# Optimization experiments

Hardware: AMD Instinct MI355X
Metric: run time of the kernel (lower is better)

## Reference

```python
import jax, jax.numpy as jnp
import numpy as np

N = 100000   # num_nodes
E = 1250000  # num_edges
D = 64       # embedding_dim
L = 3        # num_layers


def setup_inputs() -> dict:
    key = jax.random.key(0)
    k1, k2, k3, k4 = jax.random.split(key, 4)
    edge_index = jax.random.randint(k1, (2, E), 0, N, dtype=jnp.int64)
    edge_label_index = jax.random.randint(k2, (2, E), 0, N, dtype=jnp.int64)
    # xavier_uniform init of Embedding(N, D)
    bound = float(np.sqrt(6.0 / (N + D)))
    emb_weight = jax.random.uniform(k3, (N, D), jnp.float32, -bound, bound)
    alpha = jnp.full((L + 1,), 1.0 / (L + 1), dtype=jnp.float32)
    return {"edge_index": edge_index, "edge_label_index": edge_label_index,
            "emb_weight": emb_weight, "alpha": alpha}


def reference(edge_index, edge_label_index, emb_weight, alpha):
    src, dst = edge_index[0], edge_index[1]
    n = emb_weight.shape[0]
    # gcn_norm (LGConv, no self-loops): deg over destination, sym normalization
    deg = jax.ops.segment_sum(jnp.ones(src.shape[0], emb_weight.dtype), dst, num_segments=n)
    dis = jnp.where(deg > 0, jax.lax.rsqrt(jnp.where(deg > 0, deg, 1.0)), 0.0)
    w = dis[src] * dis[dst]  # [E]

    weights = jax.nn.softmax(alpha)  # [L+1]
    x = emb_weight
    out = x * weights[0]
    for i in range(L):
        # LGConv: out[dst] += norm * x[src]
        x = jax.ops.segment_sum(w[:, None] * x[src], dst, num_segments=n)
        out = out + x * weights[i + 1]

    # predict_link_embedding: per-edge dot product
    return (out[edge_label_index[0]] * out[edge_label_index[1]]).sum(axis=-1)
```

## Files before the change

kernel.cpp:

```cpp
#include <hip/hip_runtime.h>
#include <math.h>

#define DIM 64
#define PART_T 4096
#define BK_SHIFT 9
#define BK_SPAN 512
#define BK_CAP 8192
#define BK_PAD 2048
#define BK_REG (BK_CAP + BK_PAD)

typedef _Float16 half8 __attribute__((ext_vector_type(8)));


__device__ __forceinline__ half8 shfl_xor_h8(half8 v, int mask) {
    int4 iv;
    __builtin_memcpy(&iv, &v, 16);
    iv.x = __shfl_xor(iv.x, mask, 64);
    iv.y = __shfl_xor(iv.y, mask, 64);
    iv.z = __shfl_xor(iv.z, mask, 64);
    iv.w = __shfl_xor(iv.w, mask, 64);
    half8 r;
    __builtin_memcpy(&r, &iv, 16);
    return r;
}

__device__ __forceinline__ half8 dpp_ror8_h8(half8 v) {
    int4 iv;
    __builtin_memcpy(&iv, &v, 16);
    int4 r;
    r.x = __builtin_amdgcn_update_dpp(0, iv.x, 0x128, 0xF, 0xF, true);
    r.y = __builtin_amdgcn_update_dpp(0, iv.y, 0x128, 0xF, 0xF, true);
    r.z = __builtin_amdgcn_update_dpp(0, iv.z, 0x128, 0xF, 0xF, true);
    r.w = __builtin_amdgcn_update_dpp(0, iv.w, 0x128, 0xF, 0xF, true);
    half8 out;
    __builtin_memcpy(&out, &r, 16);
    return out;
}

__device__ __forceinline__ float dpp_sum8_f32(float v) {
    int x = __float_as_int(v);
    v += __int_as_float(__builtin_amdgcn_update_dpp(0, x, 0xB1, 0xF, 0xF, true));
    x = __float_as_int(v);
    v += __int_as_float(__builtin_amdgcn_update_dpp(0, x, 0x4E, 0xF, 0xF, true));
    x = __float_as_int(v);
    v += __int_as_float(__builtin_amdgcn_update_dpp(0, x, 0x141, 0xF, 0xF, true));
    return v;
}

__device__ __forceinline__ int wave_incl_scan(int v) {
    int lane = threadIdx.x & 63;
    #pragma unroll
    for (int d = 1; d < 64; d <<= 1) {
        int n = __shfl_up(v, d, 64);
        if (lane >= d) v += n;
    }
    return v;
}

__device__ __forceinline__ int block_scan_excl(int v, int* wsum) {
    int incl = wave_incl_scan(v);
    int w = threadIdx.x >> 6;
    if ((threadIdx.x & 63) == 63) wsum[w] = incl;
    __syncthreads();
    int offset = 0;
    #pragma unroll
    for (int i = 0; i < 3; ++i) offset += (i < w) ? wsum[i] : 0;
    return offset + incl - v;
}


__global__ void init_kernel(int* __restrict__ gcursor, int K) {
    int t = threadIdx.x;
    if (t < K) gcursor[t] = t * BK_CAP;
}


__global__ void part_kernel(const int* __restrict__ src, const int* __restrict__ dst,
                            int* __restrict__ gcursor, unsigned int* __restrict__ part,
                            int E, int K) {
    __shared__ unsigned int tmp_rec[PART_T];
    __shared__ unsigned int reord[PART_T];
    __shared__ unsigned char tmp_bkt[PART_T];
    __shared__ unsigned char tmp_bkt2[PART_T];
    __shared__ int hist[256];
    __shared__ int lstart[256];
    __shared__ int cursor[256];
    __shared__ int gbase[256];
    __shared__ int wsum[4];
    int t = threadIdx.x;
    int tile = blockIdx.x * PART_T;
    int n = E - tile; if (n > PART_T) n = PART_T;

    hist[t] = 0;
    __syncthreads();

    for (int i = t; i < n; i += 256) {
        int s = src[tile + i];
        int d = dst[tile + i];
        int b = d >> BK_SHIFT;
        tmp_rec[i] = (unsigned int)s | ((unsigned int)(d & (BK_SPAN - 1)) << 17);
        tmp_bkt[i] = (unsigned char)b;
        atomicAdd(&hist[b], 1);
    }
    __syncthreads();

    int hv = hist[t];
    int excl = block_scan_excl(hv, wsum);
    lstart[t] = excl;
    cursor[t] = excl;
    if (t < K && hv > 0) gbase[t] = atomicAdd(&gcursor[t], hv);
    __syncthreads();

    for (int i = t; i < n; i += 256) {
        int b = tmp_bkt[i];
        int r = atomicAdd(&cursor[b], 1);
        reord[r] = tmp_rec[i];
        tmp_bkt2[r] = (unsigned char)b;
    }
    __syncthreads();

    for (int i = t; i < n; i += 256) {
        int b = tmp_bkt2[i];
        part[gbase[b] + (i - lstart[b])] = reord[i];
    }
}


__global__ void csr_kernel(const unsigned int* __restrict__ part, const int* __restrict__ gcursor,
                           int2* __restrict__ prange, int* __restrict__ csr_src,
                           float* __restrict__ dis, int N) {
    __shared__ int h[BK_SPAN];
    __shared__ int pfx[BK_SPAN + 1];
    __shared__ int wsum[4];
    int b = blockIdx.x;
    int t = threadIdx.x;
    int pbase = b * BK_CAP;
    int cnt   = gcursor[b] - pbase;
    int qbase = b * BK_REG;
    int nodeBase = b << BK_SHIFT;

    h[t] = 0; h[t + 256] = 0;
    __syncthreads();

    for (int j = t; j < cnt; j += 256) {
        unsigned int rec = part[pbase + j];
        atomicAdd(&h[rec >> 17], 1);
    }
    __syncthreads();

    int d0 = h[2 * t], d1 = h[2 * t + 1];
    {
        int i0 = nodeBase + 2 * t, i1 = i0 + 1;
        if (i0 < N) dis[i0] = d0 > 0 ? 1.0f / sqrtf((float)d0) : 0.0f;
        if (i1 < N) dis[i1] = d1 > 0 ? 1.0f / sqrtf((float)d1) : 0.0f;
    }
    int p0 = (d0 + 3) & ~3;
    int p1 = (d1 + 3) & ~3;
    int excl = block_scan_excl(p0 + p1, wsum);
    pfx[2 * t]     = excl;
    pfx[2 * t + 1] = excl + p0;
    h[2 * t]       = excl;
    h[2 * t + 1]   = excl + p0;
    if (t == 255) pfx[BK_SPAN] = excl + p0 + p1;
    __syncthreads();

    #pragma unroll
    for (int k = 0; k < 2; ++k) {
        int i = t + k * 256;
        int idx = nodeBase + i;
        if (idx < N) prange[idx] = make_int2(qbase + pfx[i], qbase + pfx[i + 1]);
    }
    __syncthreads();

    for (int j = t; j < cnt; j += 256) {
        unsigned int rec = part[pbase + j];
        int dl = (int)(rec >> 17);
        int s  = (int)(rec & 0x1FFFFu);
        int p = atomicAdd(&h[dl], 1);
        csr_src[qbase + p] = s;
    }
    __syncthreads();

    #pragma unroll
    for (int k = 0; k < 2; ++k) {
        int i = t + k * 256;
        int endp = pfx[i + 1];
        for (int p = h[i]; p < endp; ++p) csr_src[qbase + p] = N;
    }
}


__global__ void conv_kernel(const float* __restrict__ emb, const float* __restrict__ dis,
                            half8* __restrict__ g0, half8* __restrict__ g1,
                            half8* __restrict__ g2, int n8, int N) {
    int i = blockIdx.x * blockDim.x + threadIdx.x;
    if (i < 8) {
        half8 z = (half8)(_Float16)0;
        g0[(size_t)N * 8 + i] = z;
        g1[(size_t)N * 8 + i] = z;
        g2[(size_t)N * 8 + i] = z;
    }
    if (i >= n8) return;
    int v = i >> 3;
    float d = dis[v];
    const float4* e4 = (const float4*)emb;
    float4 a = e4[2 * i], b = e4[2 * i + 1];
    half8 h;
    h[0] = (_Float16)(d * a.x); h[1] = (_Float16)(d * a.y);
    h[2] = (_Float16)(d * a.z); h[3] = (_Float16)(d * a.w);
    h[4] = (_Float16)(d * b.x); h[5] = (_Float16)(d * b.y);
    h[6] = (_Float16)(d * b.z); h[7] = (_Float16)(d * b.w);
    g0[i] = h;
}


__device__ __forceinline__ void softmax4(const float* __restrict__ alpha, float* w) {
    float a0 = alpha[0], a1 = alpha[1], a2 = alpha[2], a3 = alpha[3];
    float m = fmaxf(fmaxf(a0, a1), fmaxf(a2, a3));
    float e0 = expf(a0 - m), e1 = expf(a1 - m), e2 = expf(a2 - m), e3 = expf(a3 - m);
    float s = 1.0f / (e0 + e1 + e2 + e3);
    w[0] = e0 * s; w[1] = e1 * s; w[2] = e2 * s; w[3] = e3 * s;
}

__global__ void spmm_kernel(const int2* __restrict__ prange, const int* __restrict__ csr_src,
                            const float* __restrict__ dis,
                            const half8* __restrict__ gin, half8* __restrict__ gout, int N) {
    int lane = threadIdx.x & 63;
    int wave = blockIdx.x * (blockDim.x >> 6) + (threadIdx.x >> 6);
    int v = wave * 2 + (lane >> 5);
    int slot = (lane >> 3) & 3;
    int sub  = lane & 7;
    bool valid = v < N;
    int beg = 0, end = 0;
    if (valid) { int2 pr = prange[v]; beg = pr.x; end = pr.y; }
    const int4* csr4 = (const int4*)csr_src;
    half8 acc0 = (half8)(_Float16)0;
    half8 acc1 = (half8)(_Float16)0;
    for (int j = beg + slot * 4; j < end; j += 16) {
        int4 c = csr4[j >> 2];
        acc0 = acc0 + gin[c.x * 8 + sub];
        acc1 = acc1 + gin[c.y * 8 + sub];
        acc0 = acc0 + gin[c.z * 8 + sub];
        acc1 = acc1 + gin[c.w * 8 + sub];
    }
    half8 acc = acc0 + acc1;
    acc = acc + dpp_ror8_h8(acc);
    acc = acc + shfl_xor_h8(acc, 16);
    if (valid && (lane & 31) < 8) {
        float d = dis[v];
        float d2 = d * d;
        half8 o;
        #pragma unroll
        for (int k = 0; k < 8; ++k) o[k] = (_Float16)(d2 * (float)acc[k]);
        gout[v * 8 + sub] = o;
    }
}

__global__ void spmm_final_kernel(const int2* __restrict__ prange, const int* __restrict__ csr_src,
                                  const float* __restrict__ dis,
                                  const float* __restrict__ emb, const half8* __restrict__ g1,
                                  const half8* __restrict__ g2, half8* __restrict__ out,
                                  const float* __restrict__ alpha, int N) {
    int lane = threadIdx.x & 63;
    int wave = blockIdx.x * (blockDim.x >> 6) + (threadIdx.x >> 6);
    int v = wave * 2 + (lane >> 5);
    int slot = (lane >> 3) & 3;
    int sub  = lane & 7;
    bool valid = v < N;
    int beg = 0, end = 0;
    if (valid) { int2 pr = prange[v]; beg = pr.x; end = pr.y; }
    const int4* csr4 = (const int4*)csr_src;
    half8 acc0 = (half8)(_Float16)0;
    half8 acc1 = (half8)(_Float16)0;
    for (int j = beg + slot * 4; j < end; j += 16) {
        int4 c = csr4[j >> 2];
        acc0 = acc0 + g2[c.x * 8 + sub];
        acc1 = acc1 + g2[c.y * 8 + sub];
        acc0 = acc0 + g2[c.z * 8 + sub];
        acc1 = acc1 + g2[c.w * 8 + sub];
    }
    half8 acc = acc0 + acc1;
    acc = acc + dpp_ror8_h8(acc);
    acc = acc + shfl_xor_h8(acc, 16);
    if (valid && (lane & 31) < 8) {
        float w[4];
        softmax4(alpha, w);
        float d  = dis[v];
        float iv = d > 0.0f ? 1.0f / d : 0.0f;
        const float4* e4 = (const float4*)emb;
        float4 ea = e4[v * 16 + sub * 2];
        float4 eb = e4[v * 16 + sub * 2 + 1];
        half8 h1 = g1[v * 8 + sub];
        half8 h2 = g2[v * 8 + sub];
        float ef[8] = {ea.x, ea.y, ea.z, ea.w, eb.x, eb.y, eb.z, eb.w};
        half8 o;
        #pragma unroll
        for (int k = 0; k < 8; ++k) {
            float x1 = (float)h1[k] * iv;
            float x2 = (float)h2[k] * iv;
            float x3 = d * (float)acc[k];
            float val = w[0] * ef[k] + w[1] * x1 + w[2] * x2 + w[3] * x3;
            o[k] = (_Float16)val;
        }
        out[v * 8 + sub] = o;
    }
}

__global__ void dot_kernel(const int* __restrict__ a, const int* __restrict__ b,
                           const half8* __restrict__ out, float* __restrict__ res, int E) {
    long long g = (long long)blockIdx.x * blockDim.x + threadIdx.x;
    int e   = (int)(g >> 3);
    int sub = (int)(g & 7);
    if (e >= E) return;
    int ia = a[e];
    int ib = b[e];
    half8 va = out[ia * 8 + sub];
    half8 vb = out[ib * 8 + sub];
#if __has_builtin(__builtin_amdgcn_fdot2)
    float v = 0.f;
    v = __builtin_amdgcn_fdot2(__builtin_shufflevector(va, va, 0, 1),
                               __builtin_shufflevector(vb, vb, 0, 1), v, false);
    v = __builtin_amdgcn_fdot2(__builtin_shufflevector(va, va, 2, 3),
                               __builtin_shufflevector(vb, vb, 2, 3), v, false);
    v = __builtin_amdgcn_fdot2(__builtin_shufflevector(va, va, 4, 5),
                               __builtin_shufflevector(vb, vb, 4, 5), v, false);
    v = __builtin_amdgcn_fdot2(__builtin_shufflevector(va, va, 6, 7),
                               __builtin_shufflevector(vb, vb, 6, 7), v, false);
#else
    float v = 0.f;
    #pragma unroll
    for (int k = 0; k < 8; ++k) v += (float)va[k] * (float)vb[k];
#endif
    v = dpp_sum8_f32(v);
    if (sub == 0) res[e] = v;
}


static inline size_t align256(size_t x) { return (x + 255) & ~(size_t)255; }

extern "C" void kernel_launch(void* const* d_in, const int* in_sizes, int n_in,
                              void* d_out, int out_size, void* d_ws, size_t ws_size,
                              hipStream_t stream) {
    const int* edge_index = (const int*)d_in[0];
    const int* edge_label = (const int*)d_in[1];
    const float* emb      = (const float*)d_in[2];
    const float* alpha    = (const float*)d_in[3];

    const int E = in_sizes[0] / 2;
    const int N = in_sizes[2] / DIM;
    const int K = (N + BK_SPAN - 1) >> BK_SHIFT;

    const int* src = edge_index;
    const int* dst = edge_index + E;
    const int* la  = edge_label;
    const int* lb  = edge_label + E;

    char* ws = (char*)d_ws;
    size_t off = 0;
    float* dis     = (float*)(ws + off); off = align256(off + (size_t)N * 4);
    int2*  prange  = (int2*)(ws + off);  off = align256(off + (size_t)N * 8);
    int*   gcursor = (int*)(ws + off);   off = align256(off + (size_t)256 * 4);
    unsigned int* part = (unsigned int*)(ws + off); off = align256(off + (size_t)K * BK_CAP * 4);
    int*   csr_src = (int*)(ws + off);   off = align256(off + (size_t)K * BK_REG * 4);
    half8* g0      = (half8*)(ws + off); off = align256(off + (size_t)(N + 1) * DIM * 2);
    half8* g1      = (half8*)(ws + off); off = align256(off + (size_t)(N + 1) * DIM * 2);
    half8* g2      = (half8*)(ws + off); off = align256(off + (size_t)(N + 1) * DIM * 2);
    half8* outbuf  = g0;
    (void)ws_size;

    const int B = 256;
    const int gridT = (E + PART_T - 1) / PART_T;

    init_kernel<<<1, B, 0, stream>>>(gcursor, K);

    part_kernel<<<gridT, B, 0, stream>>>(src, dst, gcursor, part, E, K);

    csr_kernel<<<K, B, 0, stream>>>(part, gcursor, prange, csr_src, dis, N);

    const int n8 = N * DIM / 8;
    conv_kernel<<<(n8 + B - 1) / B, B, 0, stream>>>(emb, dis, g0, g1, g2, n8, N);

    const int nodesPerBlock = (B / 64) * 2;
    const int gridS = (N + nodesPerBlock - 1) / nodesPerBlock;
    spmm_kernel<<<gridS, B, 0, stream>>>(prange, csr_src, dis, g0, g1, N);
    spmm_kernel<<<gridS, B, 0, stream>>>(prange, csr_src, dis, g1, g2, N);
    spmm_final_kernel<<<gridS, B, 0, stream>>>(prange, csr_src, dis, emb, g1, g2,
                                               outbuf, alpha, N);

    const long long dthreads = (long long)E * 8;
    const int gridD = (int)((dthreads + B - 1) / B);
    dot_kernel<<<gridD, B, 0, stream>>>(la, lb, outbuf, (float*)d_out, E);
}
```

Before: 232.5 us.

## Replace bucket partition CSR build with global atomic degree count and placement

Replaces the two-pass shared-memory bucket partition (part_kernel + csr_kernel) with a global atomic degree histogram, a per-bucket prefix kernel fused with the fp16 embedding conversion, and an atomic scatter placement of sources into CSR slots. This removes the intermediate partition buffer and one pass over the edges, and folds the separate conversion kernel into the prefix kernel. In exchange it relies on 1.25M global atomics over random destinations, twice, which may contend more than the shared-memory version. Neighbor order within a row becomes nondeterministic, and the fixed 10240-entry region per 512-node bucket could overflow if degrees are skewed.

```diff
diff --git a/kernel.cpp b/kernel.cpp
--- a/kernel.cpp
+++ b/kernel.cpp
@@ -2,12 +2,9 @@
 #include <math.h>
 
 #define DIM 64
-#define PART_T 4096
 #define BK_SHIFT 9
 #define BK_SPAN 512
-#define BK_CAP 8192
-#define BK_PAD 2048
-#define BK_REG (BK_CAP + BK_PAD)
+#define BK_REG 10240
 
 typedef _Float16 half8 __attribute__((ext_vector_type(8)));
 
@@ -69,98 +66,52 @@
 }
 
 
-__global__ void init_kernel(int* __restrict__ gcursor, int K) {
-    int t = threadIdx.x;
-    if (t < K) gcursor[t] = t * BK_CAP;
-}
-
-
-__global__ void part_kernel(const int* __restrict__ src, const int* __restrict__ dst,
-                            int* __restrict__ gcursor, unsigned int* __restrict__ part,
-                            int E, int K) {
-    __shared__ unsigned int tmp_rec[PART_T];
-    __shared__ unsigned int reord[PART_T];
-    __shared__ unsigned char tmp_bkt[PART_T];
-    __shared__ unsigned char tmp_bkt2[PART_T];
-    __shared__ int hist[256];
-    __shared__ int lstart[256];
-    __shared__ int cursor[256];
-    __shared__ int gbase[256];
-    __shared__ int wsum[4];
-    int t = threadIdx.x;
-    int tile = blockIdx.x * PART_T;
-    int n = E - tile; if (n > PART_T) n = PART_T;
-
-    hist[t] = 0;
-    __syncthreads();
-
-    for (int i = t; i < n; i += 256) {
-        int s = src[tile + i];
-        int d = dst[tile + i];
-        int b = d >> BK_SHIFT;
-        tmp_rec[i] = (unsigned int)s | ((unsigned int)(d & (BK_SPAN - 1)) << 17);
-        tmp_bkt[i] = (unsigned char)b;
-        atomicAdd(&hist[b], 1);
-    }
-    __syncthreads();
-
-    int hv = hist[t];
-    int excl = block_scan_excl(hv, wsum);
-    lstart[t] = excl;
-    cursor[t] = excl;
-    if (t < K && hv > 0) gbase[t] = atomicAdd(&gcursor[t], hv);
-    __syncthreads();
-
-    for (int i = t; i < n; i += 256) {
-        int b = tmp_bkt[i];
-        int r = atomicAdd(&cursor[b], 1);
-        reord[r] = tmp_rec[i];
-        tmp_bkt2[r] = (unsigned char)b;
-    }
-    __syncthreads();
-
-    for (int i = t; i < n; i += 256) {
-        int b = tmp_bkt2[i];
-        part[gbase[b] + (i - lstart[b])] = reord[i];
-    }
-}
-
-
-__global__ void csr_kernel(const unsigned int* __restrict__ part, const int* __restrict__ gcursor,
-                           int2* __restrict__ prange, int* __restrict__ csr_src,
-                           float* __restrict__ dis, int N) {
-    __shared__ int h[BK_SPAN];
+__global__ void zero_kernel(int* __restrict__ degcur, half8* __restrict__ g0,
+                            half8* __restrict__ g1, half8* __restrict__ g2, int N) {
+    int i = blockIdx.x * blockDim.x + threadIdx.x;
+    if (i < N) degcur[i] = 0;
+    if (blockIdx.x == 0 && threadIdx.x < 8) {
+        half8 z = (half8)(_Float16)0;
+        g0[(size_t)N * 8 + threadIdx.x] = z;
+        g1[(size_t)N * 8 + threadIdx.x] = z;
+        g2[(size_t)N * 8 + threadIdx.x] = z;
+    }
+}
+
+
+__global__ void deg_kernel(const int* __restrict__ dst, int* __restrict__ degcur, int E) {
+    int e = blockIdx.x * blockDim.x + threadIdx.x;
+    if (e < E) atomicAdd(&degcur[dst[e]], 1);
+}
+
+
+__global__ void prefix_conv_kernel(int* __restrict__ degcur, float* __restrict__ dis,
+                                   int2* __restrict__ prange, int* __restrict__ csr_src,
+                                   const float* __restrict__ emb, half8* __restrict__ g0,
+                                   int N) {
     __shared__ int pfx[BK_SPAN + 1];
+    __shared__ float sdis[BK_SPAN];
     __shared__ int wsum[4];
     int b = blockIdx.x;
     int t = threadIdx.x;
-    int pbase = b * BK_CAP;
-    int cnt   = gcursor[b] - pbase;
+    int nodeBase = b << BK_SHIFT;
     int qbase = b * BK_REG;
-    int nodeBase = b << BK_SHIFT;
-
-    h[t] = 0; h[t + 256] = 0;
-    __syncthreads();
-
-    for (int j = t; j < cnt; j += 256) {
-        unsigned int rec = part[pbase + j];
-        atomicAdd(&h[rec >> 17], 1);
-    }
-    __syncthreads();
-
-    int d0 = h[2 * t], d1 = h[2 * t + 1];
-    {
-        int i0 = nodeBase + 2 * t, i1 = i0 + 1;
-        if (i0 < N) dis[i0] = d0 > 0 ? 1.0f / sqrtf((float)d0) : 0.0f;
-        if (i1 < N) dis[i1] = d1 > 0 ? 1.0f / sqrtf((float)d1) : 0.0f;
-    }
+
+    int i0 = nodeBase + 2 * t, i1 = i0 + 1;
+    int d0 = (i0 < N) ? degcur[i0] : 0;
+    int d1 = (i1 < N) ? degcur[i1] : 0;
+    float f0 = d0 > 0 ? rsqrtf((float)d0) : 0.0f;
+    float f1 = d1 > 0 ? rsqrtf((float)d1) : 0.0f;
+    if (i0 < N) dis[i0] = f0;
+    if (i1 < N) dis[i1] = f1;
+    sdis[2 * t] = f0;
+    sdis[2 * t + 1] = f1;
+
     int p0 = (d0 + 3) & ~3;
     int p1 = (d1 + 3) & ~3;
     int excl = block_scan_excl(p0 + p1, wsum);
     pfx[2 * t]     = excl;
     pfx[2 * t + 1] = excl + p0;
-    h[2 * t]       = excl;
-    h[2 * t + 1]   = excl + p0;
     if (t == 255) pfx[BK_SPAN] = excl + p0 + p1;
     __syncthreads();
 
@@ -168,49 +119,44 @@
     for (int k = 0; k < 2; ++k) {
         int i = t + k * 256;
         int idx = nodeBase + i;
-        if (idx < N) prange[idx] = make_int2(qbase + pfx[i], qbase + pfx[i + 1]);
-    }
-    __syncthreads();
-
-    for (int j = t; j < cnt; j += 256) {
-        unsigned int rec = part[pbase + j];
-        int dl = (int)(rec >> 17);
-        int s  = (int)(rec & 0x1FFFFu);
-        int p = atomicAdd(&h[dl], 1);
-        csr_src[qbase + p] = s;
-    }
-    __syncthreads();
-
-    #pragma unroll
-    for (int k = 0; k < 2; ++k) {
-        int i = t + k * 256;
-        int endp = pfx[i + 1];
-        for (int p = h[i]; p < endp; ++p) csr_src[qbase + p] = N;
-    }
-}
-
-
-__global__ void conv_kernel(const float* __restrict__ emb, const float* __restrict__ dis,
-                            half8* __restrict__ g0, half8* __restrict__ g1,
-                            half8* __restrict__ g2, int n8, int N) {
-    int i = blockIdx.x * blockDim.x + threadIdx.x;
-    if (i < 8) {
-        half8 z = (half8)(_Float16)0;
-        g0[(size_t)N * 8 + i] = z;
-        g1[(size_t)N * 8 + i] = z;
-        g2[(size_t)N * 8 + i] = z;
-    }
-    if (i >= n8) return;
-    int v = i >> 3;
-    float d = dis[v];
+        if (idx < N) {
+            int s  = qbase + pfx[i];
+            int e2 = qbase + pfx[i + 1];
+            prange[idx] = make_int2(s, e2);
+            int dd = degcur[idx];
+            degcur[idx] = s;
+            for (int p = s + dd; p < e2; ++p) csr_src[p] = N;
+        }
+    }
+
     const float4* e4 = (const float4*)emb;
-    float4 a = e4[2 * i], b = e4[2 * i + 1];
-    half8 h;
-    h[0] = (_Float16)(d * a.x); h[1] = (_Float16)(d * a.y);
-    h[2] = (_Float16)(d * a.z); h[3] = (_Float16)(d * a.w);
-    h[4] = (_Float16)(d * b.x); h[5] = (_Float16)(d * b.y);
-    h[6] = (_Float16)(d * b.z); h[7] = (_Float16)(d * b.w);
-    g0[i] = h;
+    int nloc = N - nodeBase;
+    if (nloc > BK_SPAN) nloc = BK_SPAN;
+    int lim = nloc * 8;
+    for (int j = t; j < lim; j += 256) {
+        int r = j >> 3;
+        int v = nodeBase + r;
+        float dv = sdis[r];
+        float4 a = e4[(size_t)v * 16 + (size_t)(j & 7) * 2];
+        float4 c = e4[(size_t)v * 16 + (size_t)(j & 7) * 2 + 1];
+        half8 h;
+        h[0] = (_Float16)(dv * a.x); h[1] = (_Float16)(dv * a.y);
+        h[2] = (_Float16)(dv * a.z); h[3] = (_Float16)(dv * a.w);
+        h[4] = (_Float16)(dv * c.x); h[5] = (_Float16)(dv * c.y);
+        h[6] = (_Float16)(dv * c.z); h[7] = (_Float16)(dv * c.w);
+        g0[(size_t)v * 8 + (j & 7)] = h;
+    }
+}
+
+
+__global__ void place_kernel(const int* __restrict__ src, const int* __restrict__ dst,
+                             int* __restrict__ degcur, int* __restrict__ csr_src, int E) {
+    int e = blockIdx.x * blockDim.x + threadIdx.x;
+    if (e >= E) return;
+    int s = src[e];
+    int d = dst[e];
+    int pos = atomicAdd(&degcur[d], 1);
+    csr_src[pos] = s;
 }
 
 
@@ -359,8 +305,7 @@
     size_t off = 0;
     float* dis     = (float*)(ws + off); off = align256(off + (size_t)N * 4);
     int2*  prange  = (int2*)(ws + off);  off = align256(off + (size_t)N * 8);
-    int*   gcursor = (int*)(ws + off);   off = align256(off + (size_t)256 * 4);
-    unsigned int* part = (unsigned int*)(ws + off); off = align256(off + (size_t)K * BK_CAP * 4);
+    int*   degcur  = (int*)(ws + off);   off = align256(off + (size_t)N * 4);
     int*   csr_src = (int*)(ws + off);   off = align256(off + (size_t)K * BK_REG * 4);
     half8* g0      = (half8*)(ws + off); off = align256(off + (size_t)(N + 1) * DIM * 2);
     half8* g1      = (half8*)(ws + off); off = align256(off + (size_t)(N + 1) * DIM * 2);
@@ -369,16 +314,16 @@
     (void)ws_size;
 
     const int B = 256;
-    const int gridT = (E + PART_T - 1) / PART_T;
-
-    init_kernel<<<1, B, 0, stream>>>(gcursor, K);
-
-    part_kernel<<<gridT, B, 0, stream>>>(src, dst, gcursor, part, E, K);
-
-    csr_kernel<<<K, B, 0, stream>>>(part, gcursor, prange, csr_src, dis, N);
-
-    const int n8 = N * DIM / 8;
-    conv_kernel<<<(n8 + B - 1) / B, B, 0, stream>>>(emb, dis, g0, g1, g2, n8, N);
+    const int gridE = (E + B - 1) / B;
+    const int gridN = (N + B - 1) / B;
+
+    zero_kernel<<<gridN, B, 0, stream>>>(degcur, g0, g1, g2, N);
+
+    deg_kernel<<<gridE, B, 0, stream>>>(dst, degcur, E);
+
+    prefix_conv_kernel<<<K, B, 0, stream>>>(degcur, dis, prange, csr_src, emb, g0, N);
+
+    place_kernel<<<gridE, B, 0, stream>>>(src, dst, degcur, csr_src, E);
 
     const int nodesPerBlock = (B / 64) * 2;
     const int gridS = (N + nodesPerBlock - 1) / nodesPerBlock;
```

Measured after the change: 346.7 us. 49.1% more time.
